# Performance work log

Measured on AMD Instinct MI355X. Metric: run time of the kernel, lower is better.

The kernel has to match this reference:

```python
import jax, jax.numpy as jnp
import numpy as np

DESC_DIM = 128


def setup_inputs() -> dict:
    key = jax.random.key(0)
    # [B=1, desc_dim+1, H, W] dense Unet output: 128 descriptor channels + 1 heatmap channel
    features = jax.random.normal(key, (1, DESC_DIM + 1, 1024, 1024), dtype=jnp.float32)
    return {
        "features": features,
        "orig_w": 1024,
        "orig_h": 1024,
        "max_keypoints": 2048,
        "window": 5,
    }


def reference(features, orig_w, orig_h, max_keypoints, window):
    # DISK.detect + DISK.compute (inference path):
    # max-pool NMS on heatmap, keep positives inside original image bounds,
    # take top max_keypoints by score, gather + L2-normalize descriptors.
    D = features.shape[1] - 1
    heatmap = features[0, D]            # [H, W]
    desc = features[0, :D]              # [D, H, W]
    H, W = heatmap.shape

    # local-max NMS: equality with 5x5 max pool (ties measure-zero for float data)
    pooled = jax.lax.reduce_window(
        heatmap, -jnp.inf, jax.lax.max,
        window_dimensions=(window, window), window_strides=(1, 1), padding="SAME")
    ys = jnp.arange(H)[:, None]
    xs = jnp.arange(W)[None, :]
    in_bounds = (xs <= orig_w - 1) & (ys <= orig_h - 1)  # 'valid' filter in detect()
    mask = (heatmap == pooled) & (heatmap > 0.0) & in_bounds  # cutoff=0.0

    # replace nonzero + kthvalue + argsort with masked top-k (jit-friendly, same math)
    flat = jnp.where(mask, heatmap, -jnp.inf).reshape(-1)  # [H*W]
    scores, idx = jax.lax.top_k(flat, max_keypoints)       # [K], [K]
    y = idx // W
    x = idx % W
    keypoints = jnp.stack([x, y], axis=-1).astype(jnp.float32)  # [K, 2] (x, y)

    d = desc.reshape(D, -1)[:, idx].T                      # [K, D] gather
    d = d / jnp.maximum(jnp.linalg.norm(d, axis=-1, keepdims=True), 1e-12)  # F.normalize

    valid = jnp.isfinite(scores)  # padding indicator when fewer than K detections
    return keypoints, scores, d, valid
```

## Files before the change

### kernel.cpp

```cpp
#include <hip/hip_runtime.h>
#include <stdint.h>
#include <math.h>

#define WIDTH  1024
#define HEIGHT 1024
#define DDIM   128
#define TOPK   2048
#define CAP    131072
#define SELCAP 4096

#define HIST_OFF 64
#define KEYS_OFF (HIST_OFF + 65536 * 4)
#define SEL_OFF  (KEYS_OFF + CAP * 8)
#define SIDX_OFF (SEL_OFF + SELCAP * 8)

__global__ __launch_bounds__(1024) void find_candidates(
        const float* __restrict__ feat,
        const int* __restrict__ p_ow, const int* __restrict__ p_oh,
        unsigned int* __restrict__ hdr,
        unsigned int* __restrict__ hist,
        unsigned long long* __restrict__ keys) {
    const int x = threadIdx.x;
    const int y = blockIdx.x;
    const float* hm = feat + (size_t)DDIM * WIDTH * HEIGHT;

    __shared__ unsigned long long lkeys[256];
    __shared__ unsigned int lcnt, lbase;
    if (x == 0) lcnt = 0u;
    __syncthreads();

    float c = hm[y * WIDTH + x];
    if ((c > 0.0f) && (x <= p_ow[0] - 1) && (y <= p_oh[0] - 1)) {
        int xm2 = max(x - 2, 0), xm1 = max(x - 1, 0);
        int xp1 = min(x + 1, WIDTH - 1), xp2 = min(x + 2, WIDTH - 1);
        int ym2 = max(y - 2, 0), ym1 = max(y - 1, 0);
        int yp1 = min(y + 1, HEIGHT - 1), yp2 = min(y + 2, HEIGHT - 1);
        const float* r0 = hm + ym1 * WIDTH;
        const float* r1 = hm + y   * WIDTH;
        const float* r2 = hm + yp1 * WIDTH;
        float m = fmaxf(fmaxf(fmaxf(r0[xm1], r0[x]), fmaxf(r0[xp1], r1[xm1])),
                        fmaxf(fmaxf(r1[xp1], r2[xm1]), fmaxf(r2[x], r2[xp1])));
        if (m <= c) {
            const float* ra = hm + ym2 * WIDTH;
            const float* rb = hm + yp2 * WIDTH;
            float m2 = fmaxf(fmaxf(fmaxf(ra[xm2], ra[xm1]), fmaxf(ra[x], ra[xp1])), ra[xp2]);
            m2 = fmaxf(m2, fmaxf(fmaxf(rb[xm2], rb[xm1]), fmaxf(fmaxf(rb[x], rb[xp1]), rb[xp2])));
            m2 = fmaxf(m2, fmaxf(fmaxf(r0[xm2], r0[xp2]), fmaxf(r1[xm2], r1[xp2])));
            m2 = fmaxf(m2, fmaxf(r2[xm2], r2[xp2]));
            if (m2 <= c) {
                unsigned int idx = (unsigned int)(y * WIDTH + x);
                unsigned long long key =
                    ((unsigned long long)__float_as_uint(c) << 32) |
                    (unsigned long long)(~idx);
                unsigned int p = atomicAdd(&lcnt, 1u);
                if (p < 256u) lkeys[p] = key;
            }
        }
    }
    __syncthreads();
    if (x == 0) lbase = atomicAdd(&hdr[0], lcnt);
    __syncthreads();
    unsigned int n = lcnt < 256u ? lcnt : 256u;
    unsigned int base = lbase;
    for (unsigned int i = x; i < n; i += blockDim.x) {
        unsigned long long k = lkeys[i];
        if (base + i < CAP) keys[base + i] = k;
        atomicAdd(&hist[(unsigned int)(k >> 48)], 1u);
    }
}

__global__ __launch_bounds__(1024) void scan_hist(
        unsigned int* __restrict__ hdr,
        const unsigned int* __restrict__ hist) {
    __shared__ unsigned int part[1024];
    const int tid = threadIdx.x;
    const unsigned int base = (unsigned int)tid * 64u;
    unsigned int s = 0;
    #pragma unroll 8
    for (int j = 0; j < 64; ++j) s += hist[base + j];
    part[tid] = s;
    __syncthreads();
    for (int d = 1; d < 1024; d <<= 1) {
        unsigned int v = (tid + d < 1024) ? part[tid + d] : 0u;
        __syncthreads();
        part[tid] += v;
        __syncthreads();
    }
    unsigned int N = hdr[0]; if (N > CAP) N = CAP;
    unsigned int target = N < TOPK ? N : TOPK;
    if (tid == 0) { hdr[3] = target; if (target == 0) hdr[2] = 0u; }
    if (target == 0) return;
    unsigned int St = part[tid];
    unsigned int Sn = (tid < 1023) ? part[tid + 1] : 0u;
    if (St >= target && Sn < target) {
        unsigned int above = Sn;
        unsigned int B = base;
        for (int b = (int)base + 63; b >= (int)base; --b) {
            unsigned int h = hist[b];
            if (above + h >= target) { B = (unsigned int)b; break; }
            above += h;
        }
        hdr[2] = B;
    }
}

__global__ void filter_keys(unsigned int* __restrict__ hdr,
                            const unsigned long long* __restrict__ keys,
                            unsigned long long* __restrict__ sel) {
    unsigned int N = hdr[0]; if (N > CAP) N = CAP;
    unsigned long long B = (unsigned long long)hdr[2];
    unsigned int stride = gridDim.x * blockDim.x;
    for (unsigned int i = blockIdx.x * blockDim.x + threadIdx.x; i < N; i += stride) {
        unsigned long long k = keys[i];
        if ((k >> 48) >= B) {
            unsigned int p = atomicAdd(&hdr[1], 1u);
            if (p < SELCAP) sel[p] = k;
        }
    }
}

__global__ __launch_bounds__(1024) void sort_emit(
        const unsigned int* __restrict__ hdr,
        const unsigned long long* __restrict__ sel,
        float* __restrict__ out_kp, float* __restrict__ out_sc,
        float* __restrict__ out_vd, unsigned int* __restrict__ sidx) {
    __shared__ unsigned long long sk[SELCAP];
    const int tid = threadIdx.x;
    unsigned int M = hdr[1]; if (M > SELCAP) M = SELCAP;
    unsigned int KK = hdr[3];
    for (unsigned int i = tid; i < SELCAP; i += 1024) sk[i] = (i < M) ? sel[i] : 0ull;
    __syncthreads();
    for (unsigned int size = 2; size <= SELCAP; size <<= 1) {
        for (unsigned int str = size >> 1; str > 0; str >>= 1) {
            for (unsigned int i = tid; i < SELCAP; i += 1024) {
                unsigned int j = i ^ str;
                if (j > i) {
                    unsigned long long a = sk[i], b = sk[j];
                    bool desc = ((i & size) == 0);
                    if (desc ? (a < b) : (a > b)) { sk[i] = b; sk[j] = a; }
                }
            }
            __syncthreads();
        }
    }
    for (unsigned int r = tid; r < TOPK; r += 1024) {
        unsigned long long k = sk[r];
        bool live = (r < KK);
        unsigned int idx = ~(unsigned int)(k & 0xFFFFFFFFull);
        out_kp[2 * r + 0] = live ? (float)(idx & (WIDTH - 1)) : 0.0f;
        out_kp[2 * r + 1] = live ? (float)(idx >> 10) : 0.0f;
        out_sc[r] = live ? __uint_as_float((unsigned int)(k >> 32)) : -INFINITY;
        out_vd[r] = live ? 1.0f : 0.0f;
        sidx[r]   = live ? idx : 0u;
    }
}

__global__ __launch_bounds__(128) void gather_desc(
        const float* __restrict__ feat,
        const unsigned int* __restrict__ sidx,
        float* __restrict__ out_d) {
    int kp = blockIdx.x;
    int c  = threadIdx.x;
    unsigned int idx = sidx[kp];
    float v = feat[(size_t)c * (WIDTH * HEIGHT) + idx];
    float s = v * v;
    #pragma unroll
    for (int off = 32; off > 0; off >>= 1) s += __shfl_down(s, off, 64);
    __shared__ float sw[2];
    if ((c & 63) == 0) sw[c >> 6] = s;
    __syncthreads();
    float norm = fmaxf(sqrtf(sw[0] + sw[1]), 1e-12f);
    out_d[(size_t)kp * DDIM + c] = v / norm;
}

extern "C" void kernel_launch(void* const* d_in, const int* in_sizes, int n_in,
                              void* d_out, int out_size, void* d_ws, size_t ws_size,
                              hipStream_t stream) {
    const float* feat = (const float*)d_in[0];
    const int* p_ow = (const int*)d_in[1];
    const int* p_oh = (const int*)d_in[2];

    float* out = (float*)d_out;
    float* out_kp = out;
    float* out_sc = out + 2 * TOPK;
    float* out_d  = out + 3 * TOPK;
    float* out_vd = out + 3 * TOPK + TOPK * DDIM;

    unsigned int* hdr  = (unsigned int*)d_ws;
    unsigned int* hist = (unsigned int*)((char*)d_ws + HIST_OFF);
    unsigned long long* keys = (unsigned long long*)((char*)d_ws + KEYS_OFF);
    unsigned long long* sel  = (unsigned long long*)((char*)d_ws + SEL_OFF);
    unsigned int* sidx = (unsigned int*)((char*)d_ws + SIDX_OFF);

    hipMemsetAsync(d_ws, 0, KEYS_OFF, stream);

    find_candidates<<<HEIGHT, 1024, 0, stream>>>(feat, p_ow, p_oh, hdr, hist, keys);
    scan_hist<<<1, 1024, 0, stream>>>(hdr, hist);
    filter_keys<<<128, 256, 0, stream>>>(hdr, keys, sel);
    sort_emit<<<1, 1024, 0, stream>>>(hdr, sel, out_kp, out_sc, out_vd, sidx);
    gather_desc<<<TOPK, DDIM, 0, stream>>>(feat, sidx, out_d);
}
```

Baseline: 697.7 us.

## Fuse histogram scan, key filtering and bitonic sort into one block kernel

Merges scan_hist, filter_keys and sort_emit into a single one-block kernel. The threshold and selected count now live in shared memory instead of global header words, which removes two kernel launches and a global round trip through the sel buffer. The filter pass now runs on a single 1024-thread block rather than 128 blocks, so it has less parallelism when there are many candidates. gather_desc is also reworked to use one wavefront per keypoint with two channels per lane and a shuffle-xor reduction, which drops the shared-memory sync.

```diff
diff --git a/kernel.cpp b/kernel.cpp
--- a/kernel.cpp
+++ b/kernel.cpp
@@ -11,8 +11,7 @@
 
 #define HIST_OFF 64
 #define KEYS_OFF (HIST_OFF + 65536 * 4)
-#define SEL_OFF  (KEYS_OFF + CAP * 8)
-#define SIDX_OFF (SEL_OFF + SELCAP * 8)
+#define SIDX_OFF (KEYS_OFF + CAP * 8)
 
 __global__ __launch_bounds__(1024) void find_candidates(
         const float* __restrict__ feat,
@@ -69,16 +68,24 @@
     }
 }
 
-__global__ __launch_bounds__(1024) void scan_hist(
-        unsigned int* __restrict__ hdr,
-        const unsigned int* __restrict__ hist) {
+__global__ __launch_bounds__(1024) void select_emit(
+        const unsigned int* __restrict__ hdr,
+        const unsigned int* __restrict__ hist,
+        const unsigned long long* __restrict__ keys,
+        float* __restrict__ out_kp, float* __restrict__ out_sc,
+        float* __restrict__ out_vd, unsigned int* __restrict__ sidx) {
+    __shared__ unsigned long long sk[SELCAP];
     __shared__ unsigned int part[1024];
+    __shared__ unsigned int scnt;
+    __shared__ unsigned int sB;
     const int tid = threadIdx.x;
+
     const unsigned int base = (unsigned int)tid * 64u;
     unsigned int s = 0;
     #pragma unroll 8
     for (int j = 0; j < 64; ++j) s += hist[base + j];
     part[tid] = s;
+    if (tid == 0) { scnt = 0u; sB = 0u; }
     __syncthreads();
     for (int d = 1; d < 1024; d <<= 1) {
         unsigned int v = (tid + d < 1024) ? part[tid + d] : 0u;
@@ -87,49 +94,34 @@
         __syncthreads();
     }
     unsigned int N = hdr[0]; if (N > CAP) N = CAP;
-    unsigned int target = N < TOPK ? N : TOPK;
-    if (tid == 0) { hdr[3] = target; if (target == 0) hdr[2] = 0u; }
-    if (target == 0) return;
-    unsigned int St = part[tid];
-    unsigned int Sn = (tid < 1023) ? part[tid + 1] : 0u;
-    if (St >= target && Sn < target) {
-        unsigned int above = Sn;
-        unsigned int B = base;
-        for (int b = (int)base + 63; b >= (int)base; --b) {
-            unsigned int h = hist[b];
-            if (above + h >= target) { B = (unsigned int)b; break; }
-            above += h;
+    const unsigned int target = N < TOPK ? N : TOPK;
+    if (target != 0) {
+        unsigned int St = part[tid];
+        unsigned int Sn = (tid < 1023) ? part[tid + 1] : 0u;
+        if (St >= target && Sn < target) {
+            unsigned int above = Sn;
+            unsigned int B = base;
+            for (int b = (int)base + 63; b >= (int)base; --b) {
+                unsigned int h = hist[b];
+                if (above + h >= target) { B = (unsigned int)b; break; }
+                above += h;
+            }
+            sB = B;
         }
-        hdr[2] = B;
     }
-}
+    for (unsigned int i = tid; i < SELCAP; i += 1024) sk[i] = 0ull;
+    __syncthreads();
 
-__global__ void filter_keys(unsigned int* __restrict__ hdr,
-                            const unsigned long long* __restrict__ keys,
-                            unsigned long long* __restrict__ sel) {
-    unsigned int N = hdr[0]; if (N > CAP) N = CAP;
-    unsigned long long B = (unsigned long long)hdr[2];
-    unsigned int stride = gridDim.x * blockDim.x;
-    for (unsigned int i = blockIdx.x * blockDim.x + threadIdx.x; i < N; i += stride) {
+    const unsigned long long B = (unsigned long long)sB;
+    for (unsigned int i = tid; i < N; i += 1024) {
         unsigned long long k = keys[i];
         if ((k >> 48) >= B) {
-            unsigned int p = atomicAdd(&hdr[1], 1u);
-            if (p < SELCAP) sel[p] = k;
+            unsigned int p = atomicAdd(&scnt, 1u);
+            if (p < SELCAP) sk[p] = k;
         }
     }
-}
+    __syncthreads();
 
-__global__ __launch_bounds__(1024) void sort_emit(
-        const unsigned int* __restrict__ hdr,
-        const unsigned long long* __restrict__ sel,
-        float* __restrict__ out_kp, float* __restrict__ out_sc,
-        float* __restrict__ out_vd, unsigned int* __restrict__ sidx) {
-    __shared__ unsigned long long sk[SELCAP];
-    const int tid = threadIdx.x;
-    unsigned int M = hdr[1]; if (M > SELCAP) M = SELCAP;
-    unsigned int KK = hdr[3];
-    for (unsigned int i = tid; i < SELCAP; i += 1024) sk[i] = (i < M) ? sel[i] : 0ull;
-    __syncthreads();
     for (unsigned int size = 2; size <= SELCAP; size <<= 1) {
         for (unsigned int str = size >> 1; str > 0; str >>= 1) {
             for (unsigned int i = tid; i < SELCAP; i += 1024) {
@@ -143,9 +135,10 @@
             __syncthreads();
         }
     }
+
     for (unsigned int r = tid; r < TOPK; r += 1024) {
         unsigned long long k = sk[r];
-        bool live = (r < KK);
+        bool live = (r < target);
         unsigned int idx = ~(unsigned int)(k & 0xFFFFFFFFull);
         out_kp[2 * r + 0] = live ? (float)(idx & (WIDTH - 1)) : 0.0f;
         out_kp[2 * r + 1] = live ? (float)(idx >> 10) : 0.0f;
@@ -155,22 +148,22 @@
     }
 }
 
-__global__ __launch_bounds__(128) void gather_desc(
+__global__ __launch_bounds__(256) void gather_desc(
         const float* __restrict__ feat,
         const unsigned int* __restrict__ sidx,
         float* __restrict__ out_d) {
-    int kp = blockIdx.x;
-    int c  = threadIdx.x;
-    unsigned int idx = sidx[kp];
-    float v = feat[(size_t)c * (WIDTH * HEIGHT) + idx];
-    float s = v * v;
+    const int lane = threadIdx.x & 63;
+    const int kp   = blockIdx.x * 4 + (threadIdx.x >> 6);
+    const unsigned int idx = sidx[kp];
+    const float* p = feat + idx;
+    float v0 = p[(size_t)lane        * (WIDTH * HEIGHT)];
+    float v1 = p[(size_t)(lane + 64) * (WIDTH * HEIGHT)];
+    float s = v0 * v0 + v1 * v1;
     #pragma unroll
-    for (int off = 32; off > 0; off >>= 1) s += __shfl_down(s, off, 64);
-    __shared__ float sw[2];
-    if ((c & 63) == 0) sw[c >> 6] = s;
-    __syncthreads();
-    float norm = fmaxf(sqrtf(sw[0] + sw[1]), 1e-12f);
-    out_d[(size_t)kp * DDIM + c] = v / norm;
+    for (int off = 32; off > 0; off >>= 1) s += __shfl_xor(s, off, 64);
+    float inv = 1.0f / fmaxf(sqrtf(s), 1e-12f);
+    out_d[(size_t)kp * DDIM + lane]      = v0 * inv;
+    out_d[(size_t)kp * DDIM + 64 + lane] = v1 * inv;
 }
 
 extern "C" void kernel_launch(void* const* d_in, const int* in_sizes, int n_in,
@@ -189,14 +182,11 @@
     unsigned int* hdr  = (unsigned int*)d_ws;
     unsigned int* hist = (unsigned int*)((char*)d_ws + HIST_OFF);
     unsigned long long* keys = (unsigned long long*)((char*)d_ws + KEYS_OFF);
-    unsigned long long* sel  = (unsigned long long*)((char*)d_ws + SEL_OFF);
     unsigned int* sidx = (unsigned int*)((char*)d_ws + SIDX_OFF);
 
     hipMemsetAsync(d_ws, 0, KEYS_OFF, stream);
 
     find_candidates<<<HEIGHT, 1024, 0, stream>>>(feat, p_ow, p_oh, hdr, hist, keys);
-    scan_hist<<<1, 1024, 0, stream>>>(hdr, hist);
-    filter_keys<<<128, 256, 0, stream>>>(hdr, keys, sel);
-    sort_emit<<<1, 1024, 0, stream>>>(hdr, sel, out_kp, out_sc, out_vd, sidx);
-    gather_desc<<<TOPK, DDIM, 0, stream>>>(feat, sidx, out_d);
+    select_emit<<<1, 1024, 0, stream>>>(hdr, hist, keys, out_kp, out_sc, out_vd, sidx);
+    gather_desc<<<TOPK / 4, 256, 0, stream>>>(feat, sidx, out_d);
 }
```

Result: no change. 705.8 us (+1.2%).
